# Kernel tuning notes

Hardware: AMD Instinct MI355X
Metric: run time of the kernel (lower is better)

The kernel has to match this reference:

```python
import jax, jax.numpy as jnp
import numpy as np

DT_MIN, DT_MAX, STAB_EPS, RMS_EPS = 1e-4, 10.0, 1e-8, 1e-6


def soft_clamp(x, mn=DT_MIN, mx=DT_MAX):
    center = (mx + mn) / 2.0
    half = (mx - mn) / 2.0
    return center + half * jnp.tanh((x - center) / half)


def setup_inputs() -> dict:
    key = jax.random.key(0)
    ks = jax.random.split(key, 8)
    B, L, D, N = 1, 4096, 1024, 16
    s = D ** -0.5
    x = jax.random.normal(ks[0], (B, L, D), jnp.float32)
    # S4D-real style init: A = -exp(A_log), rows = -(1..N)
    A_log = jnp.broadcast_to(jnp.log(jnp.arange(1, N + 1, dtype=jnp.float32)), (D, N))
    W_delta = jax.random.normal(ks[1], (D, D), jnp.float32) * s
    b_delta = jax.random.normal(ks[2], (D,), jnp.float32) * 0.1
    W_B = jax.random.normal(ks[3], (D, N), jnp.float32) * s
    W_C = jax.random.normal(ks[4], (D, N), jnp.float32) * s
    D_skip = jax.random.normal(ks[5], (D,), jnp.float32) * 0.1 + 1.0
    norm_weight = jnp.ones((D,), jnp.float32)
    return {"x": x, "A_log": A_log, "W_delta": W_delta, "b_delta": b_delta,
            "W_B": W_B, "W_C": W_C, "D_skip": D_skip, "norm_weight": norm_weight}


def reference(x, A_log, W_delta, b_delta, W_B, W_C, D_skip, norm_weight):
    # RMSNorm pre-norm
    rms = jnp.sqrt(jnp.mean(x * x, axis=-1, keepdims=True) + RMS_EPS)
    xn = norm_weight * x / rms                                  # (B, L, D)

    # input-dependent (selective) parameters
    delta = soft_clamp(jax.nn.softplus(xn @ W_delta + b_delta))  # (B, L, D)
    Bp = xn @ W_B                                               # (B, L, N)
    C = xn @ W_C                                                # (B, L, N)
    A = -jnp.exp(A_log)                                         # (D, N)

    # guarded Tustin (bilinear) discretization
    half_dA = 0.5 * delta[..., None] * A                        # (B, L, D, N)
    denom_inv = 1.0 / jnp.maximum(1.0 - half_dA, STAB_EPS)
    A_bar = (1.0 + half_dA) * denom_inv                         # (B, L, D, N)
    B_bar = jnp.sqrt(delta)[..., None] * Bp[:, :, None, :] * denom_inv
    Bx = B_bar * xn[..., None]                                  # (B, L, D, N)

    # linear recurrence h_t = A_bar_t * h_{t-1} + Bx_t ; y_t = sum_n C_t * h_t
    def step(h, inp):
        a_t, bx_t, c_t = inp
        h = a_t * h + bx_t                                      # (B, D, N)
        y_t = jnp.einsum('bdn,bn->bd', h, c_t)
        return h, y_t

    h0 = jnp.zeros((x.shape[0], A.shape[0], A.shape[1]), x.dtype)
    seq = (jnp.moveaxis(A_bar, 1, 0), jnp.moveaxis(Bx, 1, 0), jnp.moveaxis(C, 1, 0))
    _, ys = jax.lax.scan(step, h0, seq)
    y = jnp.moveaxis(ys, 0, 1) + D_skip * xn                    # skip connection
    return y
```

## Files before the change

### kernel.cpp

```cpp
#include <hip/hip_runtime.h>
#include <hip/hip_fp16.h>
#include <cmath>

typedef _Float16 half8 __attribute__((ext_vector_type(8)));
typedef _Float16 half4_t __attribute__((ext_vector_type(4)));
typedef _Float16 half2_t __attribute__((ext_vector_type(2)));
typedef float f32x4 __attribute__((ext_vector_type(4)));
typedef float f32x2 __attribute__((ext_vector_type(2)));

#define LDIM 4096
#define DDIM 1024
#define NSTATE 16
#define NCHUNK 128
#define CLEN 32

#define GLD16(g, l) __builtin_amdgcn_global_load_lds( \
    (const __attribute__((address_space(1))) void*)(g), \
    (__attribute__((address_space(3))) void*)(l), 16, 0, 0)

__global__ __launch_bounds__(256) void k_prep_norm(const float* __restrict__ x,
                                                   const float* __restrict__ nw,
                                                   const float* __restrict__ W,
                                                   const float* __restrict__ WB,
                                                   const float* __restrict__ WC,
                                                   _Float16* __restrict__ xnh,
                                                   _Float16* __restrict__ Wt,
                                                   _Float16* __restrict__ BCe) {
  const int b = blockIdx.x, t = threadIdx.x;
  if (b < 4096) {
    const int l = b;
    float4 v = ((const float4*)(x + (size_t)l * DDIM))[t];
    float ss = v.x * v.x + v.y * v.y + v.z * v.z + v.w * v.w;
#pragma unroll
    for (int off = 32; off; off >>= 1) ss += __shfl_xor(ss, off, 64);
    __shared__ float sred[4];
    if ((t & 63) == 0) sred[t >> 6] = ss;
    __syncthreads();
    float tot = sred[0] + sred[1] + sred[2] + sred[3];
    float r = rsqrtf(tot * (1.0f / (float)DDIM) + 1e-6f);
    float4 wv = ((const float4*)nw)[t];
    half4_t h;
    h[0] = (_Float16)(v.x * wv.x * r); h[1] = (_Float16)(v.y * wv.y * r);
    h[2] = (_Float16)(v.z * wv.z * r); h[3] = (_Float16)(v.w * wv.w * r);
    ((half4_t*)(xnh + (size_t)l * DDIM))[t] = h;
  } else if (b < 4352) {
    __shared__ float tile[64][65];
    const int bb = b - 4096;
    const int n0 = (bb & 15) * 64, k0 = (bb >> 4) * 64;
#pragma unroll
    for (int i = 0; i < 16; ++i) {
      int idx = t + i * 256;
      int kk = idx >> 6, nn = idx & 63;
      tile[kk][nn] = W[(size_t)(k0 + kk) * DDIM + n0 + nn];
    }
    __syncthreads();
#pragma unroll
    for (int i = 0; i < 16; ++i) {
      int idx = t + i * 256;
      int nn = idx >> 6, kk = idx & 63;
      Wt[(size_t)(n0 + nn) * DDIM + k0 + kk] = (_Float16)tile[kk][nn];
    }
  } else {
    const int by2 = b - 4352;
#pragma unroll
    for (int rr = 0; rr < 2; ++rr) {
      int r = 2 * by2 + rr;
      const float* src = (r < 16) ? WB : WC;
      int n = r & 15;
#pragma unroll
      for (int j = 0; j < 4; ++j) {
        int k = t * 4 + j;
        BCe[(size_t)r * DDIM + k] = (_Float16)src[(size_t)k * NSTATE + n];
      }
    }
  }
}

__global__ __launch_bounds__(256, 2) void k_gemm64(const _Float16* __restrict__ Ah,
                                                   const _Float16* __restrict__ Bh,
                                                   const _Float16* __restrict__ B2h,
                                                   const float* __restrict__ b_delta,
                                                   half2_t* __restrict__ sxh,
                                                   float* __restrict__ bpc) {
  __shared__ __align__(16) _Float16 As[2][128 * 64];
  __shared__ __align__(16) _Float16 Bs[2][64 * 64];
  __shared__ __align__(16) _Float16 B2s[2][32 * 64];
  const int t = threadIdx.x;
  const int w = t >> 6, lane = t & 63;
  const int quad = lane >> 4, l16 = lane & 15;
  const int wr = w >> 1, wc = w & 1;
  const int bid = blockIdx.x;
  const int bx = bid >> 5;
  const int by = (bid & 7) + ((bid >> 3) & 3) * 8;
  const int tileM = by * 128, tileN = bx * 64;
  const int srow = lane >> 3;
  const int sslot = (lane & 7) ^ srow;
  const _Float16* gA0 = Ah + (size_t)(tileM + w * 32 + srow) * DDIM + sslot * 8;
  const _Float16* gB0 = Bh + (size_t)(tileN + w * 16 + srow) * DDIM + sslot * 8;
  const _Float16* gC0 = B2h + (size_t)(w * 8 + srow) * DDIM + sslot * 8;

  f32x4 acc[4][2], acc2[4];
#pragma unroll
  for (int i = 0; i < 4; ++i) {
    acc2[i] = (f32x4){0.f, 0.f, 0.f, 0.f};
#pragma unroll
    for (int j = 0; j < 2; ++j) acc[i][j] = (f32x4){0.f, 0.f, 0.f, 0.f};
  }

  auto stage = [&](int kt, int p) {
    const int ko = kt * 64;
#pragma unroll
    for (int g = 0; g < 4; ++g)
      GLD16(gA0 + (size_t)g * 8 * DDIM + ko, &As[p][(w * 32 + g * 8) * 64]);
#pragma unroll
    for (int g = 0; g < 2; ++g)
      GLD16(gB0 + (size_t)g * 8 * DDIM + ko, &Bs[p][(w * 16 + g * 8) * 64]);
    if (bx == 0)
      GLD16(gC0 + ko, &B2s[p][(w * 8) * 64]);
  };

  stage(0, 0);
  for (int kt = 0; kt < 16; ++kt) {
    const int p = kt & 1;
    __syncthreads();
    if (kt < 15) stage(kt + 1, p ^ 1);
#pragma unroll
    for (int ks = 0; ks < 2; ++ks) {
      const int sw = ((ks * 4 + quad) ^ (l16 & 7)) * 8;
      half8 af[4], bf[2];
#pragma unroll
      for (int i = 0; i < 4; ++i)
        af[i] = *(const half8*)&As[p][(wr * 64 + i * 16 + l16) * 64 + sw];
#pragma unroll
      for (int j = 0; j < 2; ++j)
        bf[j] = *(const half8*)&Bs[p][(wc * 32 + j * 16 + l16) * 64 + sw];
#pragma unroll
      for (int i = 0; i < 4; ++i)
#pragma unroll
        for (int j = 0; j < 2; ++j)
          acc[i][j] = __builtin_amdgcn_mfma_f32_16x16x32_f16(af[i], bf[j], acc[i][j], 0, 0, 0);
      if (bx == 0) {
        half8 cf = *(const half8*)&B2s[p][(wc * 16 + l16) * 64 + sw];
#pragma unroll
        for (int i = 0; i < 4; ++i)
          acc2[i] = __builtin_amdgcn_mfma_f32_16x16x32_f16(af[i], cf, acc2[i], 0, 0, 0);
      }
    }
  }

  const float cC = 5.00005f, cH = 4.99995f, invH = 1.0f / 4.99995f;
  float bdl[2];
#pragma unroll
  for (int j = 0; j < 2; ++j) bdl[j] = b_delta[tileN + wc * 32 + j * 16 + l16];
#pragma unroll
  for (int i = 0; i < 4; ++i) {
#pragma unroll
    for (int r = 0; r < 4; ++r) {
      int row = tileM + wr * 64 + i * 16 + quad * 4 + r;
#pragma unroll
      for (int j = 0; j < 2; ++j) {
        int col = tileN + wc * 32 + j * 16 + l16;
        float z = acc[i][j][r] + bdl[j];
        float e = __expf(-fabsf(z));
        float sp = fmaxf(z, 0.f) + __logf(1.0f + e);
        float tt = (sp - cC) * invH;
        float e2 = __expf(2.0f * tt);
        float th = 1.0f - 2.0f * __builtin_amdgcn_rcpf(e2 + 1.0f);
        float dt = fmaf(cH, th, cC);
        half2_t pk;
        pk[0] = (_Float16)sqrtf(dt);
        pk[1] = Ah[(size_t)row * DDIM + col];
        sxh[(size_t)row * DDIM + col] = pk;
      }
      if (bx == 0)
        bpc[(size_t)row * 32 + wc * 16 + l16] = acc2[i][r];
    }
  }
}

__global__ __launch_bounds__(256, 8) void k_scan1(const half2_t* __restrict__ sxh,
                                                  const float* __restrict__ bpc,
                                                  const float* __restrict__ A_log,
                                                  float2* __restrict__ Ph) {
  __shared__ __align__(16) float bcs[CLEN * 32];
  const int t = threadIdx.x;
  const int q = t & 3;
  const int d = blockIdx.x * 64 + (t >> 2);
  const int c = blockIdx.y;
  ((float4*)bcs)[t] = ((const float4*)(bpc + (size_t)c * CLEN * 32))[t];
  float4 al = *(const float4*)(A_log + (size_t)d * NSTATE + q * 4);
  f32x2 halfA[2], h[2], P[2];
  halfA[0] = (f32x2){-0.5f * __expf(al.x), -0.5f * __expf(al.y)};
  halfA[1] = (f32x2){-0.5f * __expf(al.z), -0.5f * __expf(al.w)};
  h[0] = h[1] = (f32x2){0.f, 0.f};
  P[0] = P[1] = (f32x2){1.f, 1.f};
  __syncthreads();
  const half2_t* sxr = sxh + (size_t)c * CLEN * DDIM + d;
  const f32x2 one2 = {1.f, 1.f}, two2 = {2.f, 2.f}, mone2 = {-1.f, -1.f};
#pragma unroll 4
  for (int i = 0; i < CLEN; ++i) {
    half2_t sx = sxr[(size_t)i * DDIM];
    float sdv = (float)sx[0], xv = (float)sx[1];
    float dsq = sdv * sdv, sdx = sdv * xv;
    f32x2 dsq2 = {dsq, dsq}, sdx2 = {sdx, sdx};
    f32x4 bB = *(const f32x4*)&bcs[i * 32 + q * 4];
#pragma unroll
    for (int j = 0; j < 2; ++j) {
      f32x2 bb = (f32x2){bB[2 * j], bB[2 * j + 1]};
      f32x2 hd = dsq2 * halfA[j];
      f32x2 om = one2 - hd;
      f32x2 di = {__builtin_amdgcn_rcpf(om[0]), __builtin_amdgcn_rcpf(om[1])};
      f32x2 ab = __builtin_elementwise_fma(di, two2, mone2);
      h[j] = __builtin_elementwise_fma(ab, h[j], sdx2 * bb * di);
      P[j] = P[j] * ab;
    }
  }
#pragma unroll
  for (int j = 0; j < 2; ++j) {
    Ph[((size_t)c * NSTATE + q * 4 + 2 * j + 0) * DDIM + d] = make_float2(P[j][0], h[j][0]);
    Ph[((size_t)c * NSTATE + q * 4 + 2 * j + 1) * DDIM + d] = make_float2(P[j][1], h[j][1]);
  }
}

__global__ __launch_bounds__(64) void k_comb(const float2* __restrict__ Ph,
                                             float* __restrict__ Hinit) {
  const int g = blockIdx.x * 64 + threadIdx.x;
  float H = 0.f;
  for (int cb = 0; cb < NCHUNK; cb += 16) {
    float2 ph[16];
#pragma unroll
    for (int u = 0; u < 16; ++u)
      ph[u] = Ph[(size_t)(cb + u) * (DDIM * NSTATE) + g];
#pragma unroll
    for (int u = 0; u < 16; ++u) {
      Hinit[(size_t)(cb + u) * (DDIM * NSTATE) + g] = H;
      H = fmaf(ph[u].x, H, ph[u].y);
    }
  }
}

__global__ __launch_bounds__(256, 8) void k_scan2(const half2_t* __restrict__ sxh,
                                                  const float* __restrict__ bpc,
                                                  const float* __restrict__ A_log,
                                                  const float* __restrict__ Hinit,
                                                  const float* __restrict__ Dskip,
                                                  float* __restrict__ y) {
  __shared__ __align__(16) float bcs[CLEN * 32];
  const int t = threadIdx.x;
  const int q = t & 3;
  const int d = blockIdx.x * 64 + (t >> 2);
  const int c = blockIdx.y;
  ((float4*)bcs)[t] = ((const float4*)(bpc + (size_t)c * CLEN * 32))[t];
  float4 al = *(const float4*)(A_log + (size_t)d * NSTATE + q * 4);
  f32x2 halfA[2], h[2];
  halfA[0] = (f32x2){-0.5f * __expf(al.x), -0.5f * __expf(al.y)};
  halfA[1] = (f32x2){-0.5f * __expf(al.z), -0.5f * __expf(al.w)};
  const float* hb = Hinit + (size_t)c * (DDIM * NSTATE) + d;
  h[0] = (f32x2){hb[(size_t)(q * 4 + 0) * DDIM], hb[(size_t)(q * 4 + 1) * DDIM]};
  h[1] = (f32x2){hb[(size_t)(q * 4 + 2) * DDIM], hb[(size_t)(q * 4 + 3) * DDIM]};
  const float dsk = Dskip[d];
  __syncthreads();
  const half2_t* sxr = sxh + (size_t)c * CLEN * DDIM + d;
  float* yr = y + (size_t)c * CLEN * DDIM + d;
  const f32x2 one2 = {1.f, 1.f}, two2 = {2.f, 2.f}, mone2 = {-1.f, -1.f};
#pragma unroll 4
  for (int i = 0; i < CLEN; ++i) {
    half2_t sx = sxr[(size_t)i * DDIM];
    float sdv = (float)sx[0], xv = (float)sx[1];
    float dsq = sdv * sdv, sdx = sdv * xv;
    f32x2 dsq2 = {dsq, dsq}, sdx2 = {sdx, sdx};
    f32x4 bB = *(const f32x4*)&bcs[i * 32 + q * 4];
    f32x4 bC = *(const f32x4*)&bcs[i * 32 + 16 + q * 4];
    f32x2 acc = {0.f, 0.f};
#pragma unroll
    for (int j = 0; j < 2; ++j) {
      f32x2 bb = (f32x2){bB[2 * j], bB[2 * j + 1]};
      f32x2 cc = (f32x2){bC[2 * j], bC[2 * j + 1]};
      f32x2 hd = dsq2 * halfA[j];
      f32x2 om = one2 - hd;
      f32x2 di = {__builtin_amdgcn_rcpf(om[0]), __builtin_amdgcn_rcpf(om[1])};
      f32x2 ab = __builtin_elementwise_fma(di, two2, mone2);
      h[j] = __builtin_elementwise_fma(ab, h[j], sdx2 * bb * di);
      acc = __builtin_elementwise_fma(cc, h[j], acc);
    }
    float a = acc[0] + acc[1];
    a += __shfl_xor(a, 1, 64);
    a += __shfl_xor(a, 2, 64);
    if (q == 0) yr[(size_t)i * DDIM] = fmaf(dsk, xv, a);
  }
}

extern "C" void kernel_launch(void* const* d_in, const int* in_sizes, int n_in,
                              void* d_out, int out_size, void* d_ws, size_t ws_size,
                              hipStream_t stream) {
  const float* x       = (const float*)d_in[0];
  const float* A_log   = (const float*)d_in[1];
  const float* W_delta = (const float*)d_in[2];
  const float* b_delta = (const float*)d_in[3];
  const float* W_B     = (const float*)d_in[4];
  const float* W_C     = (const float*)d_in[5];
  const float* D_skip  = (const float*)d_in[6];
  const float* norm_w  = (const float*)d_in[7];
  float* y = (float*)d_out;

  char* ws = (char*)d_ws;
  const size_t MB = 1024 * 1024;
  _Float16* xnh = (_Float16*)(ws);
  _Float16* Wt  = (_Float16*)(ws + 8 * MB);
  _Float16* BCe = (_Float16*)(ws + 10 * MB);
  float*    bpc = (float*)(ws + 10 * MB + 512 * 1024);
  half2_t*  sxh = (half2_t*)(ws + 11 * MB);
  float2*   Ph  = (float2*)(ws + 27 * MB);
  float*    Hin = (float*)(ws + 43 * MB);
  (void)ws_size; (void)in_sizes; (void)n_in; (void)out_size;

  hipLaunchKernelGGL(k_prep_norm, dim3(4368), dim3(256), 0, stream,
                     x, norm_w, W_delta, W_B, W_C, xnh, Wt, BCe);
  hipLaunchKernelGGL(k_gemm64, dim3(512), dim3(256), 0, stream,
                     xnh, Wt, BCe, b_delta, sxh, bpc);
  hipLaunchKernelGGL(k_scan1, dim3(16, NCHUNK), dim3(256), 0, stream,
                     sxh, bpc, A_log, Ph);
  hipLaunchKernelGGL(k_comb, dim3(256), dim3(64), 0, stream, Ph, Hin);
  hipLaunchKernelGGL(k_scan2, dim3(16, NCHUNK), dim3(256), 0, stream,
                     sxh, bpc, A_log, Hin, D_skip, y);
}
```

Before: 158.5 us.

## Deepen GEMM pipeline to four stages with K-tile 32 and manual vmcnt waits

Restructures the fused delta/B/C GEMM main loop from a double-buffered 64-wide K tile to a four-stage ring of 32-wide K tiles, using explicit s_waitcnt vmcnt counts and raw barriers so several global-to-LDS loads stay in flight. It also changes the block-to-tile mapping to a simple row-major order and redistributes the B/C weight loads to only two waves. The aim is to hide global load latency better. The cost is twice as many barriers per K step and hand-tuned wait counts that must match the exact number of issued loads per wave.

New measurement: 162.9 us. +2.8%, slower.

```diff
diff --git a/kernel.cpp b/kernel.cpp
--- a/kernel.cpp
+++ b/kernel.cpp
@@ -17,6 +17,8 @@
 #define GLD16(g, l) __builtin_amdgcn_global_load_lds( \
     (const __attribute__((address_space(1))) void*)(g), \
     (__attribute__((address_space(3))) void*)(l), 16, 0, 0)
+
+#define WAITVM(n) asm volatile("s_waitcnt vmcnt(" #n ")" ::: "memory")
 
 __global__ __launch_bounds__(256) void k_prep_norm(const float* __restrict__ x,
                                                    const float* __restrict__ nw,
@@ -82,22 +84,24 @@
                                                    const float* __restrict__ b_delta,
                                                    half2_t* __restrict__ sxh,
                                                    float* __restrict__ bpc) {
-  __shared__ __align__(16) _Float16 As[2][128 * 64];
-  __shared__ __align__(16) _Float16 Bs[2][64 * 64];
-  __shared__ __align__(16) _Float16 B2s[2][32 * 64];
+  __shared__ __align__(16) _Float16 As[4][128 * 32];
+  __shared__ __align__(16) _Float16 Bs[4][64 * 32];
+  __shared__ __align__(16) _Float16 B2s[4][32 * 32];
   const int t = threadIdx.x;
   const int w = t >> 6, lane = t & 63;
   const int quad = lane >> 4, l16 = lane & 15;
   const int wr = w >> 1, wc = w & 1;
   const int bid = blockIdx.x;
-  const int bx = bid >> 5;
-  const int by = (bid & 7) + ((bid >> 3) & 3) * 8;
+  const int bx = bid & 15, by = bid >> 4;
   const int tileM = by * 128, tileN = bx * 64;
-  const int srow = lane >> 3;
-  const int sslot = (lane & 7) ^ srow;
-  const _Float16* gA0 = Ah + (size_t)(tileM + w * 32 + srow) * DDIM + sslot * 8;
-  const _Float16* gB0 = Bh + (size_t)(tileN + w * 16 + srow) * DDIM + sslot * 8;
-  const _Float16* gC0 = B2h + (size_t)(w * 8 + srow) * DDIM + sslot * 8;
+  const bool heavy = (bx == 0) && (w < 2);
+
+  const int r8 = lane >> 2;
+  const int ls = (lane & 3) ^ (r8 & 3);
+  const _Float16* gA0 = Ah + (size_t)(tileM + w * 32 + r8) * DDIM + ls * 8;
+  const _Float16* gA1 = Ah + (size_t)(tileM + w * 32 + 16 + r8) * DDIM + ls * 8;
+  const _Float16* gB0 = Bh + (size_t)(tileN + w * 16 + r8) * DDIM + ls * 8;
+  const _Float16* gC0 = B2h + (size_t)(w * 16 + r8) * DDIM + ls * 8;
 
   f32x4 acc[4][2], acc2[4];
 #pragma unroll
@@ -108,44 +112,48 @@
   }
 
   auto stage = [&](int kt, int p) {
-    const int ko = kt * 64;
-#pragma unroll
-    for (int g = 0; g < 4; ++g)
-      GLD16(gA0 + (size_t)g * 8 * DDIM + ko, &As[p][(w * 32 + g * 8) * 64]);
-#pragma unroll
-    for (int g = 0; g < 2; ++g)
-      GLD16(gB0 + (size_t)g * 8 * DDIM + ko, &Bs[p][(w * 16 + g * 8) * 64]);
-    if (bx == 0)
-      GLD16(gC0 + ko, &B2s[p][(w * 8) * 64]);
+    const int ko = kt * 32;
+    GLD16(gA0 + ko, &As[p][(w * 32) * 32]);
+    GLD16(gA1 + ko, &As[p][(w * 32 + 16) * 32]);
+    GLD16(gB0 + ko, &Bs[p][(w * 16) * 32]);
+    if (heavy) GLD16(gC0 + ko, &B2s[p][(w * 16) * 32]);
   };
 
-  stage(0, 0);
-  for (int kt = 0; kt < 16; ++kt) {
-    const int p = kt & 1;
-    __syncthreads();
-    if (kt < 15) stage(kt + 1, p ^ 1);
-#pragma unroll
-    for (int ks = 0; ks < 2; ++ks) {
-      const int sw = ((ks * 4 + quad) ^ (l16 & 7)) * 8;
-      half8 af[4], bf[2];
+  stage(0, 0); stage(1, 1); stage(2, 2); stage(3, 3);
+
+  const int swA = (quad ^ (l16 & 3)) * 8;
+  for (int kt = 0; kt < 32; ++kt) {
+    const int p = kt & 3;
+    if (kt <= 28)      { if (heavy) WAITVM(12); else WAITVM(9); }
+    else if (kt == 29) { if (heavy) WAITVM(8);  else WAITVM(6); }
+    else if (kt == 30) { if (heavy) WAITVM(4);  else WAITVM(3); }
+    else               { WAITVM(0); }
+    asm volatile("s_barrier" ::: "memory");
+    __builtin_amdgcn_sched_barrier(0);
+
+    half8 af[4], bf[2];
+#pragma unroll
+    for (int i = 0; i < 4; ++i)
+      af[i] = *(const half8*)&As[p][(wr * 64 + i * 16 + l16) * 32 + swA];
+#pragma unroll
+    for (int j = 0; j < 2; ++j)
+      bf[j] = *(const half8*)&Bs[p][(wc * 32 + j * 16 + l16) * 32 + swA];
+#pragma unroll
+    for (int i = 0; i < 4; ++i)
+#pragma unroll
+      for (int j = 0; j < 2; ++j)
+        acc[i][j] = __builtin_amdgcn_mfma_f32_16x16x32_f16(af[i], bf[j], acc[i][j], 0, 0, 0);
+    if (bx == 0) {
+      half8 cf = *(const half8*)&B2s[p][(wc * 16 + l16) * 32 + swA];
 #pragma unroll
       for (int i = 0; i < 4; ++i)
-        af[i] = *(const half8*)&As[p][(wr * 64 + i * 16 + l16) * 64 + sw];
-#pragma unroll
-      for (int j = 0; j < 2; ++j)
-        bf[j] = *(const half8*)&Bs[p][(wc * 32 + j * 16 + l16) * 64 + sw];
-#pragma unroll
-      for (int i = 0; i < 4; ++i)
-#pragma unroll
-        for (int j = 0; j < 2; ++j)
-          acc[i][j] = __builtin_amdgcn_mfma_f32_16x16x32_f16(af[i], bf[j], acc[i][j], 0, 0, 0);
-      if (bx == 0) {
-        half8 cf = *(const half8*)&B2s[p][(wc * 16 + l16) * 64 + sw];
-#pragma unroll
-        for (int i = 0; i < 4; ++i)
-          acc2[i] = __builtin_amdgcn_mfma_f32_16x16x32_f16(af[i], cf, acc2[i], 0, 0, 0);
-      }
-    }
+        acc2[i] = __builtin_amdgcn_mfma_f32_16x16x32_f16(af[i], cf, acc2[i], 0, 0, 0);
+    }
+
+    asm volatile("s_waitcnt lgkmcnt(0)" ::: "memory");
+    __builtin_amdgcn_sched_barrier(0);
+    asm volatile("s_barrier" ::: "memory");
+    if (kt < 28) stage(kt + 4, p);
   }
 
   const float cC = 5.00005f, cH = 4.99995f, invH = 1.0f / 4.99995f;
```
